# Optimization experiments

Hardware: AMD Instinct MI355X
Metric: run time of the kernel (lower is better)

Reference implementation:

```python
import jax, jax.numpy as jnp
import numpy as np

D_MODEL = 1024
N_HEADS = 16
HEAD_DIM = D_MODEL // N_HEADS


def setup_inputs() -> dict:
    key = jax.random.key(0)
    ks = jax.random.split(key, 9)
    B, S = 4, 2048
    scale = 1.0 / np.sqrt(D_MODEL)
    x = jax.random.normal(ks[0], (B, S, D_MODEL), dtype=jnp.float32)
    Wq = jax.random.normal(ks[1], (D_MODEL, D_MODEL), dtype=jnp.float32) * scale
    bq = jnp.zeros((D_MODEL,), dtype=jnp.float32)
    Wk = jax.random.normal(ks[2], (D_MODEL, D_MODEL), dtype=jnp.float32) * scale
    bk = jnp.zeros((D_MODEL,), dtype=jnp.float32)
    Wv = jax.random.normal(ks[3], (D_MODEL, D_MODEL), dtype=jnp.float32) * scale
    bv = jnp.zeros((D_MODEL,), dtype=jnp.float32)
    Wo = jax.random.normal(ks[4], (D_MODEL, D_MODEL), dtype=jnp.float32) * scale
    bo = jnp.zeros((D_MODEL,), dtype=jnp.float32)
    return {"x": x, "Wq": Wq, "bq": bq, "Wk": Wk, "bk": bk,
            "Wv": Wv, "bv": bv, "Wo": Wo, "bo": bo}


def reference(x, Wq, bq, Wk, bk, Wv, bv, Wo, bo):
    B, S, _ = x.shape
    # projections; weights stored as (in, out) so y = x @ W + b
    def split_heads(y):  # (B,S,D) -> (B,H,S,hd)
        return y.reshape(B, S, N_HEADS, HEAD_DIM).transpose(0, 2, 1, 3)
    q = split_heads(x @ Wq + bq)
    k = split_heads(x @ Wk + bk)
    v = split_heads(x @ Wv + bv)
    scale = 1.0 / np.sqrt(HEAD_DIM).astype(np.float32)
    attn = jnp.einsum('bhqd,bhkd->bhqk', q, k) * scale  # (B,H,S,S)
    attn = jax.nn.softmax(attn, axis=-1)
    out = jnp.einsum('bhqk,bhkd->bhqd', attn, v)  # (B,H,S,hd)
    out = out.transpose(0, 2, 1, 3).reshape(B, S, D_MODEL)
    return out @ Wo + bo
```

## Files before the change

kernel.cpp:

```cpp
#include <hip/hip_runtime.h>

#define DM 1024
#define NH 16
#define HD 64
#define SB 2048
#define BATCH 4
#define MROWS (BATCH*SB)

typedef float f32x4 __attribute__((ext_vector_type(4)));
typedef int   i32x4 __attribute__((ext_vector_type(4)));
typedef int   i32x2 __attribute__((ext_vector_type(2)));
typedef short bf16x8 __attribute__((ext_vector_type(8)));

static __device__ __forceinline__ unsigned short f2bf(float f){
  union { float f; unsigned u; } v; v.f = f;
  unsigned r = v.u + 0x7fffu + ((v.u >> 16) & 1u);
  return (unsigned short)(r >> 16);
}

static __device__ __forceinline__ unsigned cvtpk(float lo, float hi){
  unsigned d;
  asm("v_cvt_pk_bf16_f32 %0, %1, %2" : "=v"(d) : "v"(lo), "v"(hi));
  return d;
}

static __device__ __forceinline__ void mfma_16x16x32(f32x4& acc, i32x4 a, i32x4 b){
  acc = __builtin_amdgcn_mfma_f32_16x16x32_bf16(
      __builtin_bit_cast(bf16x8, a), __builtin_bit_cast(bf16x8, b), acc, 0, 0, 0);
}

#define AS1(p) ((const __attribute__((address_space(1))) void*)(unsigned long long)(const void*)(p))
#define AS3(p) ((__attribute__((address_space(3))) void*)(unsigned int)(unsigned long long)(const void*)(p))
#define GL2LDS(g, l) __builtin_amdgcn_global_load_lds(AS1(g), AS3(l), 16, 0, 0)


__global__ void prep_x(const float* __restrict__ x, unsigned short* __restrict__ xb, int n4){
  int stride = gridDim.x * blockDim.x;
  for (int i = blockIdx.x*blockDim.x + threadIdx.x; i < n4; i += stride){
    float4 v = ((const float4*)x)[i];
    ushort4 o = make_ushort4(f2bf(v.x), f2bf(v.y), f2bf(v.z), f2bf(v.w));
    ((ushort4*)xb)[i] = o;
  }
}

__global__ __launch_bounds__(256)
void prep_w(const float* __restrict__ Wq, const float* __restrict__ Wk,
            const float* __restrict__ Wv, const float* __restrict__ Wo,
            const float* __restrict__ bq, const float* __restrict__ bk,
            const float* __restrict__ bv,
            unsigned short* __restrict__ wqkvT, unsigned short* __restrict__ woT,
            float* __restrict__ biasqkv)
{
  const int z = blockIdx.z;
  const float* W = (z==0)?Wq:(z==1)?Wk:(z==2)?Wv:Wo;
  unsigned short* dst = (z<3) ? (wqkvT + (size_t)z*1024*1024) : woT;
  __shared__ unsigned short T[64*72];
  const int kt0 = blockIdx.x*64, nt0 = blockIdx.y*64;
  const int t = threadIdx.x, r = t>>3, c8 = (t&7)*8;
  #pragma unroll
  for (int p=0;p<2;p++){
    int k = kt0 + p*32 + r;
    float4 a = *(const float4*)&W[(size_t)k*1024 + nt0 + c8];
    float4 b2 = *(const float4*)&W[(size_t)k*1024 + nt0 + c8 + 4];
    unsigned short* Trow = &T[(p*32+r)*72 + c8];
    Trow[0]=f2bf(a.x);  Trow[1]=f2bf(a.y);  Trow[2]=f2bf(a.z);  Trow[3]=f2bf(a.w);
    Trow[4]=f2bf(b2.x); Trow[5]=f2bf(b2.y); Trow[6]=f2bf(b2.z); Trow[7]=f2bf(b2.w);
  }
  __syncthreads();
  #pragma unroll
  for (int p=0;p<2;p++){
    int n = p*32 + r;
    unsigned short tmp[8];
    #pragma unroll
    for (int j=0;j<8;j++) tmp[j] = T[(c8+j)*72 + n];
    *(i32x4*)&dst[(size_t)(nt0+n)*1024 + kt0 + c8] = *(const i32x4*)tmp;
  }
  if (z<3 && kt0==0 && t<64){
    const float* bb = (z==0)?bq:(z==1)?bk:bv;
    biasqkv[z*1024 + nt0 + t] = bb[nt0 + t];
  }
}


template<int QKVMODE>
__global__ __launch_bounds__(256)
void gemm_bt(const unsigned short* __restrict__ A, const unsigned short* __restrict__ Bt,
             const float* __restrict__ bias, void* __restrict__ Cout,
             unsigned short* __restrict__ Vout,
             int M, int N, int K)
{
  __shared__ __align__(16) unsigned short As[128*64];
  __shared__ __align__(16) unsigned short Bs[128*64];
  const int t = threadIdx.x;
  const int l = t & 63, w = t >> 6;
  const int m0 = blockIdx.y * 128, n0 = blockIdx.x * 128;
  const int wr = (w >> 1) * 64, wc = (w & 1) * 64;
  const int lr = l & 15, G = l >> 4;
  const int srow = l >> 3, sch = l & 7;
  const int gch = sch ^ srow;

  f32x4 acc[4][4];
  #pragma unroll
  for (int i=0;i<4;i++)
    #pragma unroll
    for (int j=0;j<4;j++) acc[i][j] = (f32x4)0.0f;

  for (int kt = 0; kt < K; kt += 64) {
    #pragma unroll
    for (int p = 0; p < 4; p++) {
      int r = p*32 + w*8 + srow;
      GL2LDS(A  + (size_t)(m0 + r)*K + kt + gch*8, &As[(p*32 + w*8)*64]);
      GL2LDS(Bt + (size_t)(n0 + r)*K + kt + gch*8, &Bs[(p*32 + w*8)*64]);
    }
    __syncthreads();
    #pragma unroll
    for (int ks=0; ks<2; ks++) {
      i32x4 af[4], bf[4];
      #pragma unroll
      for (int m=0;m<4;m++)
        af[m] = *(const i32x4*)&As[(wr + m*16 + lr)*64 + (((ks*4 + G) ^ (lr & 7))*8)];
      #pragma unroll
      for (int n=0;n<4;n++)
        bf[n] = *(const i32x4*)&Bs[(wc + n*16 + lr)*64 + (((ks*4 + G) ^ (lr & 7))*8)];
      #pragma unroll
      for (int m=0;m<4;m++)
        #pragma unroll
        for (int n=0;n<4;n++) mfma_16x16x32(acc[m][n], af[m], bf[n]);
    }
    __syncthreads();
  }

  #pragma unroll
  for (int m=0;m<4;m++) {
    const int rb = m0 + wr + m*16 + (l>>4)*4;
    #pragma unroll
    for (int n=0;n<4;n++) {
      int col = n0 + wc + n*16 + lr;
      float bvv = bias[col];
      float v0 = acc[m][n][0] + bvv, v1 = acc[m][n][1] + bvv;
      float v2 = acc[m][n][2] + bvv, v3 = acc[m][n][3] + bvv;
      if (!QKVMODE) {
        ((float*)Cout)[(size_t)(rb+0)*N + col] = v0;
        ((float*)Cout)[(size_t)(rb+1)*N + col] = v1;
        ((float*)Cout)[(size_t)(rb+2)*N + col] = v2;
        ((float*)Cout)[(size_t)(rb+3)*N + col] = v3;
      } else if (col < 2048) {
        float sc = (col < 1024) ? 0.18033688011112042f : 1.0f;
        unsigned short* C = (unsigned short*)Cout;
        C[(size_t)(rb+0)*2048 + col] = f2bf(v0*sc);
        C[(size_t)(rb+1)*2048 + col] = f2bf(v1*sc);
        C[(size_t)(rb+2)*2048 + col] = f2bf(v2*sc);
        C[(size_t)(rb+3)*2048 + col] = f2bf(v3*sc);
      } else {
        int dg = col - 2048, hh = dg >> 6, dd = dg & 63;
        int b = rb >> 11, s = rb & 2047, i = s & 63;
        int c = (((i>>2)&1)<<3) | (((i>>3)&1)<<4) | (((i>>4)&1)<<2) | (((i>>5)&1)<<5);
        size_t addr = ((size_t)((b*16 + hh)*64 + dd))*SB + (s & ~63) + c;
        i32x2 ov; ov[0] = (int)cvtpk(v0, v1); ov[1] = (int)cvtpk(v2, v3);
        *(i32x2*)&Vout[addr] = ov;
      }
    }
  }
}


__global__ __launch_bounds__(256)
void attn_fwd(const unsigned short* __restrict__ QKV2, const unsigned short* __restrict__ vT,
              unsigned short* __restrict__ O)
{
  __shared__ __align__(16) unsigned short Ks[2][64*64];
  __shared__ __align__(16) unsigned short VTs[2][64*64];
  const int t = threadIdx.x, l = t & 63, w = t >> 6;
  const int lr = l & 15;
  const int G  = l >> 4;
  const int lk = G * 8;
  const int q0 = blockIdx.x * 64;
  const int bh = blockIdx.y;
  const int b = bh >> 4, h = bh & 15;
  const size_t base2 = ((size_t)b * SB) * 2048 + (size_t)h * 64;
  const size_t vbase = (size_t)bh * 64 * SB;
  const i32x4 ONES = {0x3F803F80, 0x3F803F80, 0x3F803F80, 0x3F803F80};

  const int srow8 = (l >> 3), sch = (l & 7);

  i32x4 qf[2];
  {
    const size_t qrow = base2 + (size_t)(q0 + w*16 + lr) * 2048;
    qf[0] = *(const i32x4*)&QKV2[qrow + lk];
    qf[1] = *(const i32x4*)&QKV2[qrow + 32 + lk];
  }

  f32x4 oacc[4];
  #pragma unroll
  for (int g=0;g<4;g++) oacc[g] = (f32x4)0.0f;
  f32x4 dacc = (f32x4)0.0f;

#define STAGE(buf, kt)                                                          \
  {                                                                             \
    _Pragma("unroll")                                                           \
    for (int c=0;c<2;c++){                                                      \
      int row_ = w*16 + c*8 + srow8;                                            \
      int gch_ = sch ^ (row_ & 7);                                              \
      GL2LDS(QKV2 + base2 + 1024 + (size_t)((kt) + row_)*2048 + gch_*8,         \
             &Ks[buf][(w*16 + c*8)*64]);                                        \
      GL2LDS(vT + vbase + (size_t)row_*SB + (kt) + gch_*8,                      \
             &VTs[buf][(w*16 + c*8)*64]);                                       \
    }                                                                           \
  }

  STAGE(0, 0);
  asm volatile("s_waitcnt vmcnt(0)" ::: "memory");
  __builtin_amdgcn_s_barrier();

  int cur = 0;
  for (int kt = 0; kt < SB; kt += 64) {
    if (kt + 64 < SB) STAGE(cur^1, kt + 64);

    f32x4 sacc[4];
    #pragma unroll
    for (int n=0;n<4;n++) sacc[n] = (f32x4)0.0f;
    #pragma unroll
    for (int n=0;n<4;n++) {
      int row = n*16 + lr;
      #pragma unroll
      for (int ks=0;ks<2;ks++) {
        int chunk = ks*4 + G;
        i32x4 kf = *(const i32x4*)&Ks[cur][row*64 + ((chunk ^ (row & 7))*8)];
        mfma_16x16x32(sacc[n], kf, qf[ks]);
      }
    }

    float pr[4][4];
    #pragma unroll
    for (int n=0;n<4;n++)
      #pragma unroll
      for (int j=0;j<4;j++) pr[n][j] = __builtin_amdgcn_exp2f(sacc[n][j]);

    unsigned pbh[4][2];
    #pragma unroll
    for (int n=0;n<4;n++) {
      pbh[n][0] = cvtpk(pr[n][0], pr[n][1]);
      pbh[n][1] = cvtpk(pr[n][2], pr[n][3]);
    }

    #pragma unroll
    for (int ks=0; ks<2; ks++) {
      i32x4 pfrag;
      pfrag[0] = (int)pbh[2*ks  ][0];
      pfrag[1] = (int)pbh[2*ks  ][1];
      pfrag[2] = (int)pbh[2*ks+1][0];
      pfrag[3] = (int)pbh[2*ks+1][1];
      mfma_16x16x32(dacc, ONES, pfrag);
      #pragma unroll
      for (int g=0; g<4; g++) {
        int row = g*16 + lr;
        int chunk = ks*4 + G;
        i32x4 vf = *(const i32x4*)&VTs[cur][row*64 + ((chunk ^ (row & 7))*8)];
        mfma_16x16x32(oacc[g], vf, pfrag);
      }
    }

    if (kt + 64 < SB) {
      asm volatile("s_waitcnt vmcnt(0)" ::: "memory");
      __builtin_amdgcn_s_barrier();
    }
    cur ^= 1;
  }
#undef STAGE

  float inv = 1.0f / dacc[0];
  const size_t orow = (size_t)(b*SB + q0 + w*16 + lr)*1024 + (size_t)h*64;
  #pragma unroll
  for (int g=0; g<4; g++) {
    i32x2 ov;
    ov[0] = (int)cvtpk(oacc[g][0]*inv, oacc[g][1]*inv);
    ov[1] = (int)cvtpk(oacc[g][2]*inv, oacc[g][3]*inv);
    *(i32x2*)&O[orow + g*16 + G*4] = ov;
  }
}


extern "C" void kernel_launch(void* const* d_in, const int* in_sizes, int n_in,
                              void* d_out, int out_size, void* d_ws, size_t ws_size,
                              hipStream_t stream)
{
  const float* x  = (const float*)d_in[0];
  const float* Wq = (const float*)d_in[1];
  const float* bq = (const float*)d_in[2];
  const float* Wk = (const float*)d_in[3];
  const float* bk = (const float*)d_in[4];
  const float* Wv = (const float*)d_in[5];
  const float* bv = (const float*)d_in[6];
  const float* Wo = (const float*)d_in[7];
  const float* bo = (const float*)d_in[8];

  char* ws = (char*)d_ws;
  unsigned short* xb    = (unsigned short*)(ws);
  unsigned short* wqkvT = (unsigned short*)(ws + 16777216);
  float*          biasq = (float*)(ws + 23068672);
  unsigned short* woT   = (unsigned short*)(ws + 23080960);
  unsigned short* qkv2  = (unsigned short*)(ws + 25178112);
  unsigned short* vT    = (unsigned short*)(ws + 58732544);
  unsigned short* a2    = (unsigned short*)(ws + 75509760);

  prep_x<<<2048, 256, 0, stream>>>(x, xb, (MROWS*DM)/4);
  prep_w<<<dim3(16, 16, 4), 256, 0, stream>>>(Wq, Wk, Wv, Wo, bq, bk, bv,
                                              wqkvT, woT, biasq);

  gemm_bt<1><<<dim3(24, 64), 256, 0, stream>>>(xb, wqkvT, biasq, qkv2, vT, MROWS, 3072, 1024);
  attn_fwd<<<dim3(32, 64), 256, 0, stream>>>(qkv2, vT, a2);
  gemm_bt<0><<<dim3(8, 64), 256, 0, stream>>>(a2, woT, bo, d_out, nullptr, MROWS, 1024, 1024);
}
```

Before: 207.5 us.

## Split attention waves across key halves and query pairs with LDS reduction

Reorganizes the attention kernel's four waves into a 2x2 grid: each wave handles 32 queries (two 16-row groups) against half of each 64-key tile. Every K and V fragment read from LDS then feeds two MFMAs instead of one, halving LDS read traffic per MFMA. The two key-half partial outputs and denominators are combined through shared memory at the end. This adds an extra reduction phase and more accumulator registers, and it leaves V-fragment reads to a remapped chunk index.

```diff
diff --git a/kernel.cpp b/kernel.cpp
--- a/kernel.cpp
+++ b/kernel.cpp
@@ -168,12 +168,13 @@
 void attn_fwd(const unsigned short* __restrict__ QKV2, const unsigned short* __restrict__ vT,
               unsigned short* __restrict__ O)
 {
-  __shared__ __align__(16) unsigned short Ks[2][64*64];
-  __shared__ __align__(16) unsigned short VTs[2][64*64];
+  __shared__ __align__(16) unsigned short KV[2][2][64*64];
   const int t = threadIdx.x, l = t & 63, w = t >> 6;
   const int lr = l & 15;
   const int G  = l >> 4;
   const int lk = G * 8;
+  const int kw = w >> 1;
+  const int qw = w & 1;
   const int q0 = blockIdx.x * 64;
   const int bh = blockIdx.y;
   const int b = bh >> 4, h = bh & 15;
@@ -182,18 +183,23 @@
   const i32x4 ONES = {0x3F803F80, 0x3F803F80, 0x3F803F80, 0x3F803F80};
 
   const int srow8 = (l >> 3), sch = (l & 7);
-
-  i32x4 qf[2];
-  {
-    const size_t qrow = base2 + (size_t)(q0 + w*16 + lr) * 2048;
-    qf[0] = *(const i32x4*)&QKV2[qrow + lk];
-    qf[1] = *(const i32x4*)&QKV2[qrow + 32 + lk];
-  }
-
-  f32x4 oacc[4];
-  #pragma unroll
-  for (int g=0;g<4;g++) oacc[g] = (f32x4)0.0f;
-  f32x4 dacc = (f32x4)0.0f;
+  const int vchunk = kw*4 + (G>>1)*2 + (G&1);
+
+  i32x4 qf[2][2];
+  #pragma unroll
+  for (int qg=0; qg<2; qg++) {
+    const size_t qrow = base2 + (size_t)(q0 + qw*32 + qg*16 + lr) * 2048;
+    qf[qg][0] = *(const i32x4*)&QKV2[qrow + lk];
+    qf[qg][1] = *(const i32x4*)&QKV2[qrow + 32 + lk];
+  }
+
+  f32x4 oacc[4][2];
+  #pragma unroll
+  for (int dg=0;dg<4;dg++)
+    #pragma unroll
+    for (int qg=0;qg<2;qg++) oacc[dg][qg] = (f32x4)0.0f;
+  f32x4 dacc[2];
+  dacc[0] = (f32x4)0.0f; dacc[1] = (f32x4)0.0f;
 
 #define STAGE(buf, kt)                                                          \
   {                                                                             \
@@ -202,9 +208,9 @@
       int row_ = w*16 + c*8 + srow8;                                            \
       int gch_ = sch ^ (row_ & 7);                                              \
       GL2LDS(QKV2 + base2 + 1024 + (size_t)((kt) + row_)*2048 + gch_*8,         \
-             &Ks[buf][(w*16 + c*8)*64]);                                        \
+             &KV[buf][0][(w*16 + c*8)*64]);                                     \
       GL2LDS(vT + vbase + (size_t)row_*SB + (kt) + gch_*8,                      \
-             &VTs[buf][(w*16 + c*8)*64]);                                       \
+             &KV[buf][1][(w*16 + c*8)*64]);                                     \
     }                                                                           \
   }
 
@@ -216,48 +222,44 @@
   for (int kt = 0; kt < SB; kt += 64) {
     if (kt + 64 < SB) STAGE(cur^1, kt + 64);
 
-    f32x4 sacc[4];
-    #pragma unroll
-    for (int n=0;n<4;n++) sacc[n] = (f32x4)0.0f;
-    #pragma unroll
-    for (int n=0;n<4;n++) {
-      int row = n*16 + lr;
+    f32x4 sacc[2][2];
+    #pragma unroll
+    for (int n=0;n<2;n++)
+      #pragma unroll
+      for (int qg=0;qg<2;qg++) sacc[n][qg] = (f32x4)0.0f;
+    #pragma unroll
+    for (int n=0;n<2;n++) {
+      int row = kw*32 + n*16 + lr;
       #pragma unroll
       for (int ks=0;ks<2;ks++) {
-        int chunk = ks*4 + G;
-        i32x4 kf = *(const i32x4*)&Ks[cur][row*64 + ((chunk ^ (row & 7))*8)];
-        mfma_16x16x32(sacc[n], kf, qf[ks]);
+        i32x4 kf = *(const i32x4*)&KV[cur][0][row*64 + (((ks*4 + G) ^ (lr & 7))*8)];
+        mfma_16x16x32(sacc[n][0], kf, qf[0][ks]);
+        mfma_16x16x32(sacc[n][1], kf, qf[1][ks]);
       }
     }
 
-    float pr[4][4];
-    #pragma unroll
-    for (int n=0;n<4;n++)
-      #pragma unroll
-      for (int j=0;j<4;j++) pr[n][j] = __builtin_amdgcn_exp2f(sacc[n][j]);
-
-    unsigned pbh[4][2];
-    #pragma unroll
-    for (int n=0;n<4;n++) {
-      pbh[n][0] = cvtpk(pr[n][0], pr[n][1]);
-      pbh[n][1] = cvtpk(pr[n][2], pr[n][3]);
-    }
-
-    #pragma unroll
-    for (int ks=0; ks<2; ks++) {
-      i32x4 pfrag;
-      pfrag[0] = (int)pbh[2*ks  ][0];
-      pfrag[1] = (int)pbh[2*ks  ][1];
-      pfrag[2] = (int)pbh[2*ks+1][0];
-      pfrag[3] = (int)pbh[2*ks+1][1];
-      mfma_16x16x32(dacc, ONES, pfrag);
-      #pragma unroll
-      for (int g=0; g<4; g++) {
-        int row = g*16 + lr;
-        int chunk = ks*4 + G;
-        i32x4 vf = *(const i32x4*)&VTs[cur][row*64 + ((chunk ^ (row & 7))*8)];
-        mfma_16x16x32(oacc[g], vf, pfrag);
-      }
+    i32x4 pfrag[2];
+    #pragma unroll
+    for (int qg=0;qg<2;qg++) {
+      pfrag[qg][0] = (int)cvtpk(__builtin_amdgcn_exp2f(sacc[0][qg][0]),
+                                __builtin_amdgcn_exp2f(sacc[0][qg][1]));
+      pfrag[qg][1] = (int)cvtpk(__builtin_amdgcn_exp2f(sacc[0][qg][2]),
+                                __builtin_amdgcn_exp2f(sacc[0][qg][3]));
+      pfrag[qg][2] = (int)cvtpk(__builtin_amdgcn_exp2f(sacc[1][qg][0]),
+                                __builtin_amdgcn_exp2f(sacc[1][qg][1]));
+      pfrag[qg][3] = (int)cvtpk(__builtin_amdgcn_exp2f(sacc[1][qg][2]),
+                                __builtin_amdgcn_exp2f(sacc[1][qg][3]));
+    }
+
+    mfma_16x16x32(dacc[0], ONES, pfrag[0]);
+    mfma_16x16x32(dacc[1], ONES, pfrag[1]);
+
+    #pragma unroll
+    for (int dg=0; dg<4; dg++) {
+      int row = dg*16 + lr;
+      i32x4 vf = *(const i32x4*)&KV[cur][1][row*64 + ((vchunk ^ (lr & 7))*8)];
+      mfma_16x16x32(oacc[dg][0], vf, pfrag[0]);
+      mfma_16x16x32(oacc[dg][1], vf, pfrag[1]);
     }
 
     if (kt + 64 < SB) {
@@ -268,14 +270,35 @@
   }
 #undef STAGE
 
-  float inv = 1.0f / dacc[0];
-  const size_t orow = (size_t)(b*SB + q0 + w*16 + lr)*1024 + (size_t)h*64;
-  #pragma unroll
-  for (int g=0; g<4; g++) {
-    i32x2 ov;
-    ov[0] = (int)cvtpk(oacc[g][0]*inv, oacc[g][1]*inv);
-    ov[1] = (int)cvtpk(oacc[g][2]*inv, oacc[g][3]*inv);
-    *(i32x2*)&O[orow + g*16 + G*4] = ov;
+  __syncthreads();
+  float* fbuf = (float*)&KV[0][0][0];
+  float* dbuf = fbuf + 64*68;
+  if (kw == 1) {
+    #pragma unroll
+    for (int qg=0; qg<2; qg++) {
+      int ql = qw*32 + qg*16 + lr;
+      #pragma unroll
+      for (int dg=0; dg<4; dg++)
+        *(f32x4*)&fbuf[ql*68 + dg*16 + 4*G] = oacc[dg][qg];
+      if (G == 0) dbuf[ql] = dacc[qg][0];
+    }
+  }
+  __syncthreads();
+  if (kw == 0) {
+    #pragma unroll
+    for (int qg=0; qg<2; qg++) {
+      int ql = qw*32 + qg*16 + lr;
+      float inv = 1.0f / (dacc[qg][0] + dbuf[ql]);
+      const size_t orow = (size_t)(b*SB + q0 + ql)*1024 + (size_t)h*64;
+      #pragma unroll
+      for (int dg=0; dg<4; dg++) {
+        f32x4 s = oacc[dg][qg] + *(const f32x4*)&fbuf[ql*68 + dg*16 + 4*G];
+        i32x2 ov;
+        ov[0] = (int)cvtpk(s[0]*inv, s[1]*inv);
+        ov[1] = (int)cvtpk(s[2]*inv, s[3]*inv);
+        *(i32x2*)&O[orow + dg*16 + 4*G] = ov;
+      }
+    }
   }
 }
 
```

New measurement: 212.1 us. +2.2%, slower.
